# Kernel optimization log

Hardware: AMD Instinct MI355X
Metric: run time of the kernel (lower is better)

Reference implementation:

```python
import jax, jax.numpy as jnp
import numpy as np

EPS = 1e-9


def setup_inputs() -> dict:
    key = jax.random.key(0)
    k1, k2 = jax.random.split(key)
    B, IN, OUT = 16384, 2048, 2048
    x = jax.random.normal(k1, (B, IN), dtype=jnp.float32)
    w = jax.random.normal(k2, (OUT, IN), dtype=jnp.float32)
    # set_weight_norms_to(initial_weight_norm=0.01): rescale each row's L2 norm to 0.01
    wn = jnp.linalg.norm(w, axis=1, keepdims=True)
    weight = 0.01 * w / (wn + 1e-10)
    logprior = jnp.zeros((OUT,), dtype=jnp.float32)
    lamb = jnp.float32(4.0)  # initial_lambda
    return {"x": x, "weight": weight, "logprior": logprior, "lamb": lamb}


def reference(x, weight, logprior, lamb):
    # L2-normalize inputs per row
    x_n = x / (jnp.linalg.norm(x, axis=1, keepdims=True) + EPS)  # [B, IN]
    # L2-normalize weight rows -> cosine similarities
    W = weight / (jnp.linalg.norm(weight, axis=1, keepdims=True) + EPS)  # [OUT, IN]
    a = x_n @ W.T  # [B, OUT] cosine sims
    # RePU inhibition, triangle=False -> setpoint 0
    u = jax.nn.relu(a)
    un = u / (jnp.max(u) + EPS)  # global max normalization
    # power-law with logprior; safe power (0**lamb == 0) to keep grads clean
    pos = un > 0
    ulamb = jnp.where(pos, jnp.where(pos, un, 1.0) ** lamb, 0.0) * jnp.exp(logprior)
    y = ulamb / (jnp.sum(ulamb, axis=1, keepdims=True) + EPS)
    return y
```

## Files before the change

kernel.cpp:

```cpp
#include <hip/hip_runtime.h>
#include <hip/hip_bf16.h>

typedef unsigned short u16;
typedef __attribute__((ext_vector_type(8))) short bf16x8;
typedef __attribute__((ext_vector_type(4))) float f32x4;

#define EPSN 1e-9f


__device__ __forceinline__ u16 f2bf(float f) {
    union { float f; unsigned int u; } c; c.f = f;
    unsigned int u = c.u;
    unsigned int r = (u + 0x7FFFu + ((u >> 16) & 1u)) >> 16;
    return (u16)r;
}

__device__ __forceinline__ void load16_to_lds(const void* g, void* l) {
    __builtin_amdgcn_global_load_lds(
        (const __attribute__((address_space(1))) void*)g,
        (__attribute__((address_space(3))) void*)l,
        16, 0, 0);
}

__global__ __launch_bounds__(256) void normalize_cast2(
    const float* __restrict__ X, const float* __restrict__ W,
    u16* __restrict__ XO, u16* __restrict__ WO, int ncols, int nxrows, int nrt) {
    const int lane = threadIdx.x & 63;
    const int r = blockIdx.x * 4 + (threadIdx.x >> 6);
    if (r >= nrt) return;
    const float* src; u16* dst; size_t row;
    if (r < nxrows) { src = X; dst = XO; row = r; }
    else            { src = W; dst = WO; row = r - nxrows; }

    const float4* xr = (const float4*)(src + row * (size_t)ncols);
    const int nq = ncols >> 2;

    float4 v[8];
    float ss = 0.f;
    #pragma unroll
    for (int q = 0; q < 8; ++q) {
        int i = lane + q * 64;
        if (i < nq) {
            v[q] = xr[i];
            ss += v[q].x*v[q].x + v[q].y*v[q].y + v[q].z*v[q].z + v[q].w*v[q].w;
        }
    }
    #pragma unroll
    for (int o = 32; o > 0; o >>= 1) ss += __shfl_xor(ss, o);
    const float s = 1.f / (sqrtf(ss) + EPSN);

    ushort4* yr = (ushort4*)(dst + row * (size_t)ncols);
    #pragma unroll
    for (int q = 0; q < 8; ++q) {
        int i = lane + q * 64;
        if (i < nq) {
            ushort4 o4;
            o4.x = f2bf(v[q].x * s); o4.y = f2bf(v[q].y * s);
            o4.z = f2bf(v[q].z * s); o4.w = f2bf(v[q].w * s);
            yr[i] = o4;
        }
    }
}

#define BK 64

__global__ __launch_bounds__(256, 2) void gemm_softhebb(
    const u16* __restrict__ A, const u16* __restrict__ B,
    const float* __restrict__ logprior, const float* __restrict__ lambp,
    float* __restrict__ Ul, float* __restrict__ rowsum,
    int M, int N, int K) {
    __shared__ __align__(16) u16 lA[128 * BK];
    __shared__ __align__(16) u16 lB[128 * BK];

    const int tid  = threadIdx.x;
    const int lane = tid & 63;
    const int wm   = (tid >> 6) & 1;
    const int wn   = tid >> 7;
    const int row0 = blockIdx.y * 128;
    const int col0 = blockIdx.x * 128;

    f32x4 acc[4][4] = {};

    const u16* ap[4];
    const u16* bp[4];
    #pragma unroll
    for (int p = 0; p < 4; ++p) {
        int c = p * 256 + tid;
        int r = c >> 3;
        int o = ((c & 7) ^ (r & 7)) * 8;
        ap[p] = A + (size_t)(row0 + r) * K + o;
        bp[p] = B + (size_t)(col0 + r) * K + o;
    }

    for (int k0 = 0; k0 < K; k0 += BK) {
        #pragma unroll
        for (int p = 0; p < 4; ++p) {
            int c = p * 256 + tid;
            load16_to_lds(ap[p] + k0, &lA[c * 8]);
            load16_to_lds(bp[p] + k0, &lB[c * 8]);
        }
        __syncthreads();

        #pragma unroll
        for (int s = 0; s < 2; ++s) {
            const int pos = (((s << 2) + (lane >> 4)) ^ (lane & 7)) * 8;
            bf16x8 af[4], bfr[4];
            #pragma unroll
            for (int i = 0; i < 4; ++i) {
                int r = wm * 64 + i * 16 + (lane & 15);
                af[i] = *(const bf16x8*)&lA[r * 64 + pos];
            }
            #pragma unroll
            for (int j = 0; j < 4; ++j) {
                int r = wn * 64 + j * 16 + (lane & 15);
                bfr[j] = *(const bf16x8*)&lB[r * 64 + pos];
            }
            #pragma unroll
            for (int i = 0; i < 4; ++i)
                #pragma unroll
                for (int j = 0; j < 4; ++j)
                    acc[i][j] = __builtin_amdgcn_mfma_f32_16x16x32_bf16(
                        af[i], bfr[j], acc[i][j], 0, 0, 0);
        }
        __syncthreads();
    }

    const float lam = *lambp;
    const bool lam4 = (lam == 4.0f);
    float el[4];
    #pragma unroll
    for (int j = 0; j < 4; ++j)
        el[j] = __expf(logprior[col0 + wn * 64 + j * 16 + (lane & 15)]);

    #pragma unroll
    for (int i = 0; i < 4; ++i) {
        #pragma unroll
        for (int p = 0; p < 4; ++p) {
            const int m = row0 + wm * 64 + i * 16 + (lane >> 4) * 4 + p;
            float* outrow = Ul + (size_t)m * N + col0 + wn * 64 + (lane & 15);
            float rs = 0.f;
            #pragma unroll
            for (int j = 0; j < 4; ++j) {
                float a = acc[i][j][p];
                float u = 0.f;
                if (a > 0.f) {
                    float pw;
                    if (lam4) { float a2 = a * a; pw = a2 * a2; }
                    else      { pw = __powf(a, lam); }
                    u = pw * el[j];
                }
                outrow[j * 16] = u;
                rs += u;
            }
            rs += __shfl_xor(rs, 1);
            rs += __shfl_xor(rs, 2);
            rs += __shfl_xor(rs, 4);
            rs += __shfl_xor(rs, 8);
            if ((lane & 15) == 0) atomicAdd(&rowsum[m], rs);
        }
    }
}

__global__ __launch_bounds__(256) void finalize_row(
    float* __restrict__ Ul, const float* __restrict__ rowsum, int nq) {
    #pragma unroll
    for (int r = 0; r < 8; ++r) {
        const size_t row = (size_t)blockIdx.x * 8 + r;
        const float inv = 1.f / (rowsum[row] + EPSN);
        float4* p = (float4*)(Ul + row * (size_t)nq * 4);
        for (int i = threadIdx.x; i < nq; i += 256) {
            float4 v = p[i];
            v.x *= inv; v.y *= inv; v.z *= inv; v.w *= inv;
            p[i] = v;
        }
    }
}

static inline size_t align256(size_t x) { return (x + 255) & ~(size_t)255; }

extern "C" void kernel_launch(void* const* d_in, const int* in_sizes, int n_in,
                              void* d_out, int out_size, void* d_ws, size_t ws_size,
                              hipStream_t stream) {
    const float* x        = (const float*)d_in[0];
    const float* w        = (const float*)d_in[1];
    const float* logprior = (const float*)d_in[2];
    const float* lamb     = (const float*)d_in[3];
    const int OUT = in_sizes[2];
    const int IN  = in_sizes[1] / OUT;
    const int B   = in_sizes[0] / IN;
    float* out = (float*)d_out;

    char* ws = (char*)d_ws;
    size_t off = 0;
    u16* xn = (u16*)(ws + off);         off += align256((size_t)B * IN * sizeof(u16));
    u16* wn = (u16*)(ws + off);         off += align256((size_t)OUT * IN * sizeof(u16));
    float* rowsum = (float*)(ws + off); off += align256((size_t)B * sizeof(float));

    hipMemsetAsync(rowsum, 0, (size_t)B * sizeof(float), stream);

    const int nrt = B + OUT;
    normalize_cast2<<<(nrt + 3) / 4, 256, 0, stream>>>(x, w, xn, wn, IN, B, nrt);

    dim3 grid(OUT / 128, B / 128);
    gemm_softhebb<<<grid, 256, 0, stream>>>(xn, wn, logprior, lamb, out, rowsum, B, OUT, IN);

    finalize_row<<<B / 8, 256, 0, stream>>>(out, rowsum, OUT / 4);
}
```

Baseline: 426.7 us.

## Rewrite GEMM as 256x256 tile, 8-wave, double-buffered pipelined kernel with XCD swizzle

The GEMM moves from a 128x128 tile with 4 waves and a load-then-compute loop to a 256x256 tile with 8 waves. It double-buffers LDS and issues the next k-tile's global-to-LDS loads while MFMAs run, using explicit waitcnt, barriers and setprio. The block index is remapped in a 1D grid (wg&7)*64 + wg>>3 for chiplet locality. The goal is to hide memory latency and raise arithmetic intensity, at the cost of 128KB LDS per block and tricky synchronisation that may limit occupancy to one block per CU. The hardcoded 64 in the remap assumes a 512-block grid.

```diff
diff --git a/kernel.cpp b/kernel.cpp
--- a/kernel.cpp
+++ b/kernel.cpp
@@ -62,101 +62,154 @@
     }
 }
 
-#define BK 64
-
-__global__ __launch_bounds__(256, 2) void gemm_softhebb(
+__global__ __launch_bounds__(512, 2) void gemm_softhebb(
     const u16* __restrict__ A, const u16* __restrict__ B,
     const float* __restrict__ logprior, const float* __restrict__ lambp,
     float* __restrict__ Ul, float* __restrict__ rowsum,
     int M, int N, int K) {
-    __shared__ __align__(16) u16 lA[128 * BK];
-    __shared__ __align__(16) u16 lB[128 * BK];
+    __shared__ __align__(16) u16 lA[32768];
+    __shared__ __align__(16) u16 lB[32768];
 
     const int tid  = threadIdx.x;
     const int lane = tid & 63;
-    const int wm   = (tid >> 6) & 1;
-    const int wn   = tid >> 7;
-    const int row0 = blockIdx.y * 128;
-    const int col0 = blockIdx.x * 128;
-
-    f32x4 acc[4][4] = {};
-
-    const u16* ap[4];
-    const u16* bp[4];
-    #pragma unroll
-    for (int p = 0; p < 4; ++p) {
-        int c = p * 256 + tid;
-        int r = c >> 3;
-        int o = ((c & 7) ^ (r & 7)) * 8;
-        ap[p] = A + (size_t)(row0 + r) * K + o;
-        bp[p] = B + (size_t)(col0 + r) * K + o;
-    }
-
-    for (int k0 = 0; k0 < K; k0 += BK) {
+    const int wid  = tid >> 6;
+    const int wm   = wid >> 2;
+    const int wn   = wid & 3;
+
+    int wg = blockIdx.x;
+    wg = (wg & 7) * 64 + (wg >> 3);
+    const int ntn = N >> 8;
+    const int tm = wg / ntn, tn = wg - tm * ntn;
+    const int row0 = tm << 8, col0 = tn << 8;
+
+    const int srow = tid >> 3;
+    const int scol = ((tid & 7) ^ (srow & 7)) * 8;
+    const u16* Ab_ = A + (size_t)row0 * K;
+    const u16* Bb_ = B + (size_t)col0 * K;
+    const int nt = K >> 6;
+
+    auto stageA = [&](u16* lbase, int halfsel, int T) {
+        const int koff = (T < nt) ? (T << 6) : 0;
+        const u16* g = Ab_ + (size_t)(halfsel * 128 + srow) * K + koff + scol;
+        u16* d = lbase + halfsel * 8192 + tid * 8;
+        load16_to_lds(g, d);
+        load16_to_lds(g + (size_t)64 * K, d + 4096);
+    };
+    auto stageB = [&](u16* lbase, int halfsel, int T) {
+        const int koff = (T < nt) ? (T << 6) : 0;
+        const u16* g = Bb_ + (size_t)(halfsel * 128 + srow) * K + koff + scol;
+        u16* d = lbase + halfsel * 8192 + tid * 8;
+        load16_to_lds(g, d);
+        load16_to_lds(g + (size_t)64 * K, d + 4096);
+    };
+
+    const int ar = (wm * 64 + (lane & 15)) * 64;
+    const int br = (wn * 32 + (lane & 15)) * 64;
+    const int x7 = lane & 7;
+    const int ck = lane >> 4;
+    int kp[2];
+    kp[0] = ((0 + ck) ^ x7) * 8;
+    kp[1] = ((4 + ck) ^ x7) * 8;
+
+    f32x4 acc[2][2][4][2] = {};
+    bf16x8 af[4][2];
+
+    stageA(lA, 0, 0); stageB(lB, 0, 0); stageA(lA, 1, 0); stageB(lB, 1, 0);
+    stageA(lA + 16384, 0, 1); stageB(lB + 16384, 0, 1);
+    asm volatile("s_waitcnt vmcnt(4)" ::: "memory");
+    __builtin_amdgcn_s_barrier();
+
+    const int iters = nt >> 1;
+    for (int u = 0; u < iters; ++u) {
         #pragma unroll
-        for (int p = 0; p < 4; ++p) {
-            int c = p * 256 + tid;
-            load16_to_lds(ap[p] + k0, &lA[c * 8]);
-            load16_to_lds(bp[p] + k0, &lB[c * 8]);
-        }
-        __syncthreads();
-
-        #pragma unroll
-        for (int s = 0; s < 2; ++s) {
-            const int pos = (((s << 2) + (lane >> 4)) ^ (lane & 7)) * 8;
-            bf16x8 af[4], bfr[4];
+        for (int th = 0; th < 2; ++th) {
+            const int t   = 2 * u + th;
+            const int buf = th;
+            const u16* pA = lA + buf * 16384;
+            const u16* pB = lB + buf * 16384;
+            u16* oA = lA + (buf ^ 1) * 16384;
+            u16* oB = lB + (buf ^ 1) * 16384;
+
             #pragma unroll
-            for (int i = 0; i < 4; ++i) {
-                int r = wm * 64 + i * 16 + (lane & 15);
-                af[i] = *(const bf16x8*)&lA[r * 64 + pos];
+            for (int q = 0; q < 4; ++q) {
+                const int mh = q >> 1, nh = q & 1;
+                if (nh == 0) {
+                    #pragma unroll
+                    for (int i = 0; i < 4; ++i)
+                        #pragma unroll
+                        for (int kk = 0; kk < 2; ++kk)
+                            af[i][kk] = *(const bf16x8*)(pA + mh * 8192 + ar + i * 1024 + kp[kk]);
+                }
+                bf16x8 bfr[2][2];
+                #pragma unroll
+                for (int j = 0; j < 2; ++j)
+                    #pragma unroll
+                    for (int kk = 0; kk < 2; ++kk)
+                        bfr[j][kk] = *(const bf16x8*)(pB + nh * 8192 + br + j * 1024 + kp[kk]);
+                if      (q == 0) stageA(oA, 1, t + 1);
+                else if (q == 1) stageB(oB, 1, t + 1);
+                else if (q == 2) stageA((u16*)(lA + buf * 16384), 0, t + 2);
+                else             stageB((u16*)(lB + buf * 16384), 0, t + 2);
+                if (nh == 0) asm volatile("s_waitcnt lgkmcnt(8)" ::: "memory");
+                __builtin_amdgcn_s_barrier();
+                asm volatile("s_waitcnt lgkmcnt(0)" ::: "memory");
+                __builtin_amdgcn_s_setprio(1);
+                #pragma unroll
+                for (int i = 0; i < 4; ++i)
+                    #pragma unroll
+                    for (int j = 0; j < 2; ++j)
+                        #pragma unroll
+                        for (int kk = 0; kk < 2; ++kk)
+                            acc[mh][nh][i][j] = __builtin_amdgcn_mfma_f32_16x16x32_bf16(
+                                af[i][kk], bfr[j][kk], acc[mh][nh][i][j], 0, 0, 0);
+                __builtin_amdgcn_s_setprio(0);
+                if (q == 3) asm volatile("s_waitcnt vmcnt(4)" ::: "memory");
+                __builtin_amdgcn_s_barrier();
             }
-            #pragma unroll
-            for (int j = 0; j < 4; ++j) {
-                int r = wn * 64 + j * 16 + (lane & 15);
-                bfr[j] = *(const bf16x8*)&lB[r * 64 + pos];
-            }
-            #pragma unroll
-            for (int i = 0; i < 4; ++i)
-                #pragma unroll
-                for (int j = 0; j < 4; ++j)
-                    acc[i][j] = __builtin_amdgcn_mfma_f32_16x16x32_bf16(
-                        af[i], bfr[j], acc[i][j], 0, 0, 0);
-        }
-        __syncthreads();
-    }
+        }
+    }
+    asm volatile("s_waitcnt vmcnt(0)" ::: "memory");
 
     const float lam = *lambp;
     const bool lam4 = (lam == 4.0f);
-    float el[4];
-    #pragma unroll
-    for (int j = 0; j < 4; ++j)
-        el[j] = __expf(logprior[col0 + wn * 64 + j * 16 + (lane & 15)]);
-
-    #pragma unroll
-    for (int i = 0; i < 4; ++i) {
+    float el[2][2];
+    #pragma unroll
+    for (int nh = 0; nh < 2; ++nh)
         #pragma unroll
-        for (int p = 0; p < 4; ++p) {
-            const int m = row0 + wm * 64 + i * 16 + (lane >> 4) * 4 + p;
-            float* outrow = Ul + (size_t)m * N + col0 + wn * 64 + (lane & 15);
-            float rs = 0.f;
+        for (int j = 0; j < 2; ++j)
+            el[nh][j] = __expf(logprior[col0 + nh * 128 + wn * 32 + j * 16 + (lane & 15)]);
+
+    #pragma unroll
+    for (int mh = 0; mh < 2; ++mh) {
+        #pragma unroll
+        for (int i = 0; i < 4; ++i) {
             #pragma unroll
-            for (int j = 0; j < 4; ++j) {
-                float a = acc[i][j][p];
-                float u = 0.f;
-                if (a > 0.f) {
-                    float pw;
-                    if (lam4) { float a2 = a * a; pw = a2 * a2; }
-                    else      { pw = __powf(a, lam); }
-                    u = pw * el[j];
+            for (int p = 0; p < 4; ++p) {
+                const int m = row0 + mh * 128 + wm * 64 + i * 16 + (lane >> 4) * 4 + p;
+                float* orow = Ul + (size_t)m * N + col0 + wn * 32 + (lane & 15);
+                float rs = 0.f;
+                #pragma unroll
+                for (int nh = 0; nh < 2; ++nh) {
+                    #pragma unroll
+                    for (int j = 0; j < 2; ++j) {
+                        float a = acc[mh][nh][i][j][p];
+                        float uu = 0.f;
+                        if (a > 0.f) {
+                            float pw;
+                            if (lam4) { float a2 = a * a; pw = a2 * a2; }
+                            else      { pw = __powf(a, lam); }
+                            uu = pw * el[nh][j];
+                        }
+                        orow[nh * 128 + j * 16] = uu;
+                        rs += uu;
+                    }
                 }
-                outrow[j * 16] = u;
-                rs += u;
+                rs += __shfl_xor(rs, 1);
+                rs += __shfl_xor(rs, 2);
+                rs += __shfl_xor(rs, 4);
+                rs += __shfl_xor(rs, 8);
+                if ((lane & 15) == 0) atomicAdd(&rowsum[m], rs);
             }
-            rs += __shfl_xor(rs, 1);
-            rs += __shfl_xor(rs, 2);
-            rs += __shfl_xor(rs, 4);
-            rs += __shfl_xor(rs, 8);
-            if ((lane & 15) == 0) atomicAdd(&rowsum[m], rs);
         }
     }
 }
@@ -201,8 +254,8 @@
     const int nrt = B + OUT;
     normalize_cast2<<<(nrt + 3) / 4, 256, 0, stream>>>(x, w, xn, wn, IN, B, nrt);
 
-    dim3 grid(OUT / 128, B / 128);
-    gemm_softhebb<<<grid, 256, 0, stream>>>(xn, wn, logprior, lamb, out, rowsum, B, OUT, IN);
+    const int nblk = (B / 256) * (OUT / 256);
+    gemm_softhebb<<<nblk, 512, 0, stream>>>(xn, wn, logprior, lamb, out, rowsum, B, OUT, IN);
 
     finalize_row<<<B / 8, 256, 0, stream>>>(out, rowsum, OUT / 4);
 }
```

New measurement: 478.2 us. +12.1%, slower.
